# Kernel optimization log

Measured on AMD Instinct MI355X. Metric: run time of the kernel, lower is better.

## Reference

```python
import jax, jax.numpy as jnp
import numpy as np
from jax import lax

T, B, I, H = 512, 64, 1024, 1024
MIN_VAL, MAX_VAL = -1.0, 1.0  # ConstScalarClamp bounds for both hardtanh norm-scales


def setup_inputs() -> dict:
    key = jax.random.key(0)
    ks = jax.random.split(key, 12)
    return {
        "inputs": jax.random.normal(ks[0], (T, B, I), jnp.float32),
        "state": jax.random.normal(ks[1], (B, H), jnp.float32),
        "weight_ri": jax.random.normal(ks[2], (H, I), jnp.float32) * 0.02,
        "weight_ii": jax.random.normal(ks[3], (H, I), jnp.float32) * 0.02,
        "weight_ni": jax.random.normal(ks[4], (H, I), jnp.float32) * 0.02,
        "weight_rh": jax.random.normal(ks[5], (H, H), jnp.float32) * 0.02,
        "weight_ih": jax.random.normal(ks[6], (H, H), jnp.float32) * 0.02,
        "weight_nh": jax.random.normal(ks[7], (H, H), jnp.float32) * 0.02,
        "bias_r": jax.random.normal(ks[8], (H,), jnp.float32) * 0.02,
        "bias_i": jax.random.normal(ks[9], (H,), jnp.float32) * 0.02,
        "bias_ni": jax.random.normal(ks[10], (H,), jnp.float32) * 0.02,
        "bias_nh": jax.random.normal(ks[11], (H,), jnp.float32) * 0.02,
    }


def _clamp(x):
    return jnp.clip(x, MIN_VAL, MAX_VAL)


def reference(inputs, state, weight_ri, weight_ii, weight_ni,
              weight_rh, weight_ih, weight_nh,
              bias_r, bias_i, bias_ni, bias_nh):
    # FP quant type: weight proxies are identity, quant_sigmoid/tanh are plain
    # sigmoid/tanh, and both norm-scale QuantHardTanh ops are clamp to [-1, 1].
    h0 = _clamp(state)  # state = norm_scale_out(state) before the loop

    def step(h, x_t):
        x = _clamp(x_t)  # input_quant = norm_scale_out(inputs[i])
        rgate = jax.nn.sigmoid(x @ weight_ri.T + h @ weight_rh.T + bias_r)
        igate = jax.nn.sigmoid(x @ weight_ii.T + h @ weight_ih.T + bias_i)
        gates_ni = x @ weight_ni.T + bias_ni
        gates_nh = h @ weight_nh.T + bias_nh
        ngate = jnp.tanh(_clamp(gates_ni) + _clamp(rgate * gates_nh))
        s = _clamp(h) - ngate
        hy = ngate + _clamp(igate * s)
        return hy, hy

    last, outputs = lax.scan(step, h0, inputs)
    return outputs, last
```

## Files before the change

### kernel.cpp

```cpp
#include <hip/hip_runtime.h>
#include <hip/hip_bf16.h>
#include <cstdio>


typedef short bf16x8 __attribute__((ext_vector_type(8)));
typedef float f32x4 __attribute__((ext_vector_type(4)));
typedef int i32x4 __attribute__((ext_vector_type(4)));

#define NT 512
#define NB 64
#define NH 1024
#define NBH 65536

#define OFF_HBUF  4096UL
#define OFF_WCAT  (OFF_HBUF + 2UL * NB * NH * 4)
#define OFF_WH    (OFF_WCAT + 3UL * NH * NH * 2)
#define OFF_GR    (OFF_WH   + 3UL * NH * NH * 2)
#define OFF_GI    (OFF_GR   + (unsigned long)NT * NB * NH * 2)
#define WS_NEED   (OFF_GI   + (unsigned long)NT * NB * NH * 2)

__device__ __forceinline__ float clampf(float x) { return fminf(fmaxf(x, -1.f), 1.f); }

__device__ __forceinline__ unsigned short f2bf(float x) {
  __hip_bfloat16 h = __float2bfloat16(x);
  union { __hip_bfloat16 h; unsigned short u; } cv;
  cv.h = h;
  return cv.u;
}
__device__ __forceinline__ float bf2f(unsigned short u) {
  return __uint_as_float(((unsigned)u) << 16);
}
__device__ __forceinline__ float frcp(float x) { return __builtin_amdgcn_rcpf(x); }
__device__ __forceinline__ float fsigmoid(float x) { return frcp(1.f + __expf(-x)); }
__device__ __forceinline__ float ftanh(float z) { return 1.f - 2.f * frcp(1.f + __expf(2.f * z)); }

__device__ __forceinline__ i32x4 pack8(float4 v0, float4 v1) {
  i32x4 q;
  q[0] = (int)(f2bf(clampf(v0.x)) | ((unsigned)f2bf(clampf(v0.y)) << 16));
  q[1] = (int)(f2bf(clampf(v0.z)) | ((unsigned)f2bf(clampf(v0.w)) << 16));
  q[2] = (int)(f2bf(clampf(v1.x)) | ((unsigned)f2bf(clampf(v1.y)) << 16));
  q[3] = (int)(f2bf(clampf(v1.z)) | ((unsigned)f2bf(clampf(v1.w)) << 16));
  return q;
}

__device__ __forceinline__ void load_frags8(const unsigned short* p, i32x4 a[8]) {
  asm volatile(
      "global_load_dwordx4 %0, %8, off\n\t"
      "global_load_dwordx4 %1, %8, off offset:64\n\t"
      "global_load_dwordx4 %2, %8, off offset:128\n\t"
      "global_load_dwordx4 %3, %8, off offset:192\n\t"
      "global_load_dwordx4 %4, %8, off offset:256\n\t"
      "global_load_dwordx4 %5, %8, off offset:320\n\t"
      "global_load_dwordx4 %6, %8, off offset:384\n\t"
      "global_load_dwordx4 %7, %8, off offset:448\n\t"
      "s_waitcnt vmcnt(0)"
      : "=&v"(a[0]), "=&v"(a[1]), "=&v"(a[2]), "=&v"(a[3]),
        "=&v"(a[4]), "=&v"(a[5]), "=&v"(a[6]), "=&v"(a[7])
      : "v"(p)
      : "memory");
}
__device__ __forceinline__ void store_u32_wt(unsigned int* p, unsigned v) {
  asm volatile("global_store_dword %0, %1, off sc0 sc1" :: "v"(p), "v"(v) : "memory");
}

__global__ void k_convert_weights(const float* __restrict__ wri, const float* __restrict__ wii,
                                  const float* __restrict__ wni, const float* __restrict__ wrh,
                                  const float* __restrict__ wih, const float* __restrict__ wnh,
                                  unsigned short* __restrict__ wcat, unsigned short* __restrict__ wh) {
  const long total = 6L * 1024 * 1024;
  long stride = (long)gridDim.x * blockDim.x * 4;
  for (long i = ((long)blockIdx.x * blockDim.x + threadIdx.x) * 4; i < total; i += stride) {
    int m = (int)(i >> 20);
    long off = i & 1048575L;
    const float* srcs[6] = {wri, wii, wni, wrh, wih, wnh};
    float4 v = *(const float4*)(srcs[m] + off);
    ushort4 o;
    o.x = f2bf(v.x); o.y = f2bf(v.y); o.z = f2bf(v.z); o.w = f2bf(v.w);
    unsigned short* dst = (m < 3) ? (wcat + ((long)m << 20) + off)
                                  : (wh + ((long)(m - 3) << 20) + off);
    *(ushort4*)dst = o;
  }
}

#define BK 64
__launch_bounds__(256)
__global__ void k_gemm_x(const float* __restrict__ A,
                         const unsigned short* __restrict__ Bw,
                         unsigned short* __restrict__ gr, unsigned short* __restrict__ gi,
                         float* __restrict__ gni,
                         const float* __restrict__ br, const float* __restrict__ bi,
                         const float* __restrict__ bni) {
  __shared__ unsigned short As[128 * BK];
  __shared__ unsigned short Bs[128 * BK];

  int bid = blockIdx.x;
  int bm = bid / 24, bn = bid % 24;
  int tid = threadIdx.x;
  int lane = tid & 63, w = tid >> 6;
  int wm = w >> 1, wn = w & 1;

  long arow0 = (long)bm * 128;
  long brow0 = (long)bn * 128;

  f32x4 acc[4][4] = {};

  for (int kt = 0; kt < 1024; kt += BK) {
    __syncthreads();
#pragma unroll
    for (int it = 0; it < 4; ++it) {
      int f = it * 2048 + tid * 8;
      int r = f >> 6, c = f & 63;
      const float* ap = A + (arow0 + r) * 1024 + kt + c;
      float4 v0 = *(const float4*)ap;
      float4 v1 = *(const float4*)(ap + 4);
      i32x4 p = pack8(v0, v1);
      *(i32x4*)(&As[f]) = p;
      *(int4*)(&Bs[f]) = *(const int4*)(Bw + (brow0 + r) * 1024 + kt + c);
    }
    __syncthreads();
#pragma unroll
    for (int ks = 0; ks < 2; ++ks) {
      bf16x8 a[4], b[4];
#pragma unroll
      for (int fm = 0; fm < 4; ++fm)
        a[fm] = *(const bf16x8*)(&As[(wm * 64 + fm * 16 + (lane & 15)) * BK + ks * 32 + (lane >> 4) * 8]);
#pragma unroll
      for (int fn = 0; fn < 4; ++fn)
        b[fn] = *(const bf16x8*)(&Bs[(wn * 64 + fn * 16 + (lane & 15)) * BK + ks * 32 + (lane >> 4) * 8]);
#pragma unroll
      for (int fm = 0; fm < 4; ++fm)
#pragma unroll
        for (int fn = 0; fn < 4; ++fn)
          acc[fm][fn] = __builtin_amdgcn_mfma_f32_16x16x32_bf16(a[fm], b[fn], acc[fm][fn], 0, 0, 0);
    }
  }

  int g = bn >> 3;
  const float* bias = (g == 0) ? br : (g == 1) ? bi : bni;
#pragma unroll
  for (int fm = 0; fm < 4; ++fm) {
    long m = arow0 + wm * 64 + fm * 16 + (lane >> 4) * 4;
#pragma unroll
    for (int fn = 0; fn < 4; ++fn) {
      long n = brow0 + wn * 64 + fn * 16 + (lane & 15);
      long colg = n & 1023;
      float bv = bias[colg];
#pragma unroll
      for (int r2 = 0; r2 < 4; ++r2) {
        float v = acc[fm][fn][r2] + bv;
        long idx = (m + r2) * 1024 + colg;
        if (g == 0)      gr[idx] = f2bf(v);
        else if (g == 1) gi[idx] = f2bf(v);
        else             gni[idx] = clampf(v);
      }
    }
  }
}

__launch_bounds__(256, 1)
__global__ void k_recurrent(const unsigned short* __restrict__ wh,
                            const unsigned short* __restrict__ gr,
                            const unsigned short* __restrict__ gi,
                            const float* __restrict__ state,
                            const float* __restrict__ bias_nh,
                            unsigned int* __restrict__ hbuf,
                            float* __restrict__ out) {
  __shared__ unsigned short h_lds[8 * 1024];
  __shared__ float red[4][3][2][8][16];

  int tid = threadIdx.x;
  int lane = tid & 63, w = tid >> 6;
  int wg = blockIdx.x;
  int grp = wg >> 5;
  int slot = wg & 31;

  int klane = (lane >> 4) * 8;
  int k0 = w * 256;
  i32x4 wfi[3][2][8];
#pragma unroll
  for (int g2 = 0; g2 < 3; ++g2)
#pragma unroll
    for (int n2 = 0; n2 < 2; ++n2) {
      int col = slot * 32 + n2 * 16 + (lane & 15);
      load_frags8(wh + ((long)g2 << 20) + (long)col * 1024 + k0 + klane, wfi[g2][n2]);
    }

  int row = tid >> 5, col = tid & 31;
  long cellofs = (long)(grp * 8 + row) * 1024 + slot * 32 + col;
  float h_local = clampf(state[cellofs]);
  float bnh = bias_nh[slot * 32 + col];

#pragma unroll
  for (int c = 0; c < 4; ++c) {
    int m = c * 256 + tid;
    const float* sp = state + (long)grp * 8192 + (long)m * 8;
    float4 v0 = *(const float4*)sp;
    float4 v1 = *(const float4*)(sp + 4);
    int flat = m * 16;
    int r8 = m >> 7;
    *(i32x4*)((char*)h_lds + (flat ^ (r8 << 4))) = pack8(v0, v1);
  }

  const int rowb = (lane & 7) * 2048;
  const int colb = w * 512 + ((lane >> 4) * 16);
  const int rsw = (lane & 7) << 4;

  float grv = bf2f(gr[cellofs]);
  float giv = bf2f(gi[cellofs]);
  float gniv = out[cellofs];

  __syncthreads();

#pragma unroll 1
  for (int t = 0; t < NT; ++t) {
    f32x4 acc[3][2] = {};
#pragma unroll
    for (int s = 0; s < 8; ++s) {
      bf16x8 a = *(const bf16x8*)((const char*)h_lds + rowb + ((colb + s * 64) ^ rsw));
#pragma unroll
      for (int g2 = 0; g2 < 3; ++g2)
#pragma unroll
        for (int n2 = 0; n2 < 2; ++n2)
          acc[g2][n2] = __builtin_amdgcn_mfma_f32_16x16x32_bf16(
              a, __builtin_bit_cast(bf16x8, wfi[g2][n2][s]), acc[g2][n2], 0, 0, 0);
    }

    int rq = lane >> 4;
    if (rq < 2) {
#pragma unroll
      for (int g2 = 0; g2 < 3; ++g2)
#pragma unroll
        for (int n2 = 0; n2 < 2; ++n2)
#pragma unroll
          for (int r = 0; r < 4; ++r)
            red[w][g2][n2][rq * 4 + r][lane & 15] = acc[g2][n2][r];
    }
    __syncthreads();

    int n2c = col >> 4, cc = col & 15;
    float pr = red[0][0][n2c][row][cc] + red[1][0][n2c][row][cc]
             + red[2][0][n2c][row][cc] + red[3][0][n2c][row][cc];
    float pi = red[0][1][n2c][row][cc] + red[1][1][n2c][row][cc]
             + red[2][1][n2c][row][cc] + red[3][1][n2c][row][cc];
    float pn = red[0][2][n2c][row][cc] + red[1][2][n2c][row][cc]
             + red[2][2][n2c][row][cc] + red[3][2][n2c][row][cc];

    float rg = fsigmoid(pr + grv);
    float ig = fsigmoid(pi + giv);
    float ng = ftanh(gniv + clampf(rg * (pn + bnh)));
    float sx = clampf(h_local) - ng;
    float hy = ng + clampf(ig * sx);

    out[(long)t * NBH + cellofs] = hy;
    h_local = hy;

    unsigned tgt = (unsigned)(t + 1);
    long bank = (long)(tgt & 1) * NBH;
    store_u32_wt(hbuf + bank + cellofs, ((unsigned)f2bf(hy) << 16) | tgt);

    if (t + 1 < NT) {
      long g2ofs = (long)tgt * NBH + cellofs;
      grv = bf2f(gr[g2ofs]); giv = bf2f(gi[g2ofs]); gniv = out[g2ofs];

      const unsigned int* base = hbuf + bank + (long)grp * 8192;
      i32x4 d[8];
      for (unsigned it = 0;; ++it) {
#pragma unroll
        for (int c = 0; c < 8; ++c) {
          const unsigned int* p = base + (long)(c * 256 + tid) * 4;
          asm volatile("global_load_dwordx4 %0, %1, off sc0 sc1"
                       : "=&v"(d[c]) : "v"(p) : "memory");
        }
        asm volatile("s_waitcnt vmcnt(0)" ::: "memory");
        unsigned mn = 0xFFFFFFFFu;
#pragma unroll
        for (int c = 0; c < 8; ++c)
#pragma unroll
          for (int e = 0; e < 4; ++e)
            mn = min(mn, ((unsigned)d[c][e]) & 0xFFFFu);
        if (__all((int)(mn >= tgt)) || it > 4096u) break;
        __builtin_amdgcn_s_sleep(2);
      }
#pragma unroll
      for (int c = 0; c < 8; ++c) {
        int n = c * 256 + tid;
        int flat = n * 8;
        int r8 = n >> 8;
        int swz = flat ^ (r8 << 4);
        int2 v;
        v.x = (int)__builtin_amdgcn_perm((unsigned)d[c][1], (unsigned)d[c][0], 0x07060302u);
        v.y = (int)__builtin_amdgcn_perm((unsigned)d[c][3], (unsigned)d[c][2], 0x07060302u);
        *(int2*)((char*)h_lds + swz) = v;
      }
      __syncthreads();
    }
  }

  out[(long)NT * NBH + cellofs] = h_local;
}

extern "C" void kernel_launch(void* const* d_in, const int* in_sizes, int n_in,
                              void* d_out, int out_size, void* d_ws, size_t ws_size,
                              hipStream_t stream) {
  const float* inputs = (const float*)d_in[0];
  const float* state  = (const float*)d_in[1];
  const float* wri = (const float*)d_in[2];
  const float* wii = (const float*)d_in[3];
  const float* wni = (const float*)d_in[4];
  const float* wrh = (const float*)d_in[5];
  const float* wih = (const float*)d_in[6];
  const float* wnh = (const float*)d_in[7];
  const float* br  = (const float*)d_in[8];
  const float* bi  = (const float*)d_in[9];
  const float* bni = (const float*)d_in[10];
  const float* bnh = (const float*)d_in[11];

  if (ws_size < WS_NEED) {
    fprintf(stderr, "kernel_launch: ws too small (%zu < %lu)\n", ws_size, WS_NEED);
    return;
  }

  char* ws = (char*)d_ws;
  unsigned int*   hbuf  = (unsigned int*)(ws + OFF_HBUF);
  unsigned short* wcat  = (unsigned short*)(ws + OFF_WCAT);
  unsigned short* whp   = (unsigned short*)(ws + OFF_WH);
  unsigned short* grw   = (unsigned short*)(ws + OFF_GR);
  unsigned short* giw   = (unsigned short*)(ws + OFF_GI);
  float* out = (float*)d_out;

  hipMemsetAsync(ws, 0, OFF_WCAT, stream);
  k_convert_weights<<<512, 256, 0, stream>>>(wri, wii, wni, wrh, wih, wnh, wcat, whp);
  k_gemm_x<<<6144, 256, 0, stream>>>(inputs, wcat, grw, giw, out, br, bi, bni);
  k_recurrent<<<256, 256, 0, stream>>>(whp, grw, giw, state, bnh, hbuf, out);
}
```

Measured before the change: 1.986 ms.

## Drop per-step barrier via double-buffered reduction and per-chunk flag polling

The recurrent kernel double-buffers the cross-wave reduction array by step parity and removes the trailing __syncthreads after the h exchange. Each wave now polls only the slice of K it consumes, re-issuing loads only for chunks whose step flags are not yet ready. The hbuf flag store moves ahead of the output store, and the pre-GEMM stages the bf16 weight tile through direct global-to-LDS loads. Without the barrier, waves can read h_lds written by other waves, so correctness depends on the new mapping in which each wave writes exactly the K slice it later reads.

```diff
diff --git a/kernel.cpp b/kernel.cpp
--- a/kernel.cpp
+++ b/kernel.cpp
@@ -41,6 +41,12 @@
   q[2] = (int)(f2bf(clampf(v1.x)) | ((unsigned)f2bf(clampf(v1.y)) << 16));
   q[3] = (int)(f2bf(clampf(v1.z)) | ((unsigned)f2bf(clampf(v1.w)) << 16));
   return q;
+}
+
+__device__ __forceinline__ void gload_lds16(const void* g, void* l) {
+  __builtin_amdgcn_global_load_lds(
+      (const __attribute__((address_space(1))) void*)g,
+      (__attribute__((address_space(3))) void*)l, 16, 0, 0);
 }
 
 __device__ __forceinline__ void load_frags8(const unsigned short* p, i32x4 a[8]) {
@@ -110,12 +116,11 @@
     for (int it = 0; it < 4; ++it) {
       int f = it * 2048 + tid * 8;
       int r = f >> 6, c = f & 63;
+      gload_lds16(Bw + (brow0 + r) * 1024 + kt + c, &Bs[f]);
       const float* ap = A + (arow0 + r) * 1024 + kt + c;
       float4 v0 = *(const float4*)ap;
       float4 v1 = *(const float4*)(ap + 4);
-      i32x4 p = pack8(v0, v1);
-      *(i32x4*)(&As[f]) = p;
-      *(int4*)(&Bs[f]) = *(const int4*)(Bw + (brow0 + r) * 1024 + kt + c);
+      *(i32x4*)(&As[f]) = pack8(v0, v1);
     }
     __syncthreads();
 #pragma unroll
@@ -166,7 +171,7 @@
                             unsigned int* __restrict__ hbuf,
                             float* __restrict__ out) {
   __shared__ unsigned short h_lds[8 * 1024];
-  __shared__ float red[4][3][2][8][16];
+  __shared__ float red[2][4][3][2][8][16];
 
   int tid = threadIdx.x;
   int lane = tid & 63, w = tid >> 6;
@@ -191,14 +196,14 @@
   float bnh = bias_nh[slot * 32 + col];
 
 #pragma unroll
-  for (int c = 0; c < 4; ++c) {
-    int m = c * 256 + tid;
-    const float* sp = state + (long)grp * 8192 + (long)m * 8;
-    float4 v0 = *(const float4*)sp;
-    float4 v1 = *(const float4*)(sp + 4);
-    int flat = m * 16;
-    int r8 = m >> 7;
-    *(i32x4*)((char*)h_lds + (flat ^ (r8 << 4))) = pack8(v0, v1);
+  for (int c = 0; c < 8; ++c) {
+    const float* sp = state + (long)(grp * 8 + c) * 1024 + k0 + lane * 4;
+    float4 v = *(const float4*)sp;
+    int2 pv;
+    pv.x = (int)(f2bf(clampf(v.x)) | ((unsigned)f2bf(clampf(v.y)) << 16));
+    pv.y = (int)(f2bf(clampf(v.z)) | ((unsigned)f2bf(clampf(v.w)) << 16));
+    int flat = c * 2048 + (k0 + lane * 4) * 2;
+    *(int2*)((char*)h_lds + (flat ^ (c << 4))) = pv;
   }
 
   const int rowb = (lane & 7) * 2048;
@@ -213,6 +218,7 @@
 
 #pragma unroll 1
   for (int t = 0; t < NT; ++t) {
+    int par = t & 1;
     f32x4 acc[3][2] = {};
 #pragma unroll
     for (int s = 0; s < 8; ++s) {
@@ -233,17 +239,17 @@
         for (int n2 = 0; n2 < 2; ++n2)
 #pragma unroll
           for (int r = 0; r < 4; ++r)
-            red[w][g2][n2][rq * 4 + r][lane & 15] = acc[g2][n2][r];
+            red[par][w][g2][n2][rq * 4 + r][lane & 15] = acc[g2][n2][r];
     }
     __syncthreads();
 
     int n2c = col >> 4, cc = col & 15;
-    float pr = red[0][0][n2c][row][cc] + red[1][0][n2c][row][cc]
-             + red[2][0][n2c][row][cc] + red[3][0][n2c][row][cc];
-    float pi = red[0][1][n2c][row][cc] + red[1][1][n2c][row][cc]
-             + red[2][1][n2c][row][cc] + red[3][1][n2c][row][cc];
-    float pn = red[0][2][n2c][row][cc] + red[1][2][n2c][row][cc]
-             + red[2][2][n2c][row][cc] + red[3][2][n2c][row][cc];
+    float pr = red[par][0][0][n2c][row][cc] + red[par][1][0][n2c][row][cc]
+             + red[par][2][0][n2c][row][cc] + red[par][3][0][n2c][row][cc];
+    float pi = red[par][0][1][n2c][row][cc] + red[par][1][1][n2c][row][cc]
+             + red[par][2][1][n2c][row][cc] + red[par][3][1][n2c][row][cc];
+    float pn = red[par][0][2][n2c][row][cc] + red[par][1][2][n2c][row][cc]
+             + red[par][2][2][n2c][row][cc] + red[par][3][2][n2c][row][cc];
 
     float rg = fsigmoid(pr + grv);
     float ig = fsigmoid(pi + giv);
@@ -251,48 +257,45 @@
     float sx = clampf(h_local) - ng;
     float hy = ng + clampf(ig * sx);
 
-    out[(long)t * NBH + cellofs] = hy;
-    h_local = hy;
-
     unsigned tgt = (unsigned)(t + 1);
     long bank = (long)(tgt & 1) * NBH;
     store_u32_wt(hbuf + bank + cellofs, ((unsigned)f2bf(hy) << 16) | tgt);
+    out[(long)t * NBH + cellofs] = hy;
+    h_local = hy;
 
     if (t + 1 < NT) {
       long g2ofs = (long)tgt * NBH + cellofs;
       grv = bf2f(gr[g2ofs]); giv = bf2f(gi[g2ofs]); gniv = out[g2ofs];
 
-      const unsigned int* base = hbuf + bank + (long)grp * 8192;
+      const unsigned int* base = hbuf + bank + (long)grp * 8192 + k0 + lane * 4;
       i32x4 d[8];
-      for (unsigned it = 0;; ++it) {
-#pragma unroll
-        for (int c = 0; c < 8; ++c) {
-          const unsigned int* p = base + (long)(c * 256 + tid) * 4;
-          asm volatile("global_load_dwordx4 %0, %1, off sc0 sc1"
-                       : "=&v"(d[c]) : "v"(p) : "memory");
-        }
+      unsigned done = 0;
+      for (unsigned it2 = 0;; ++it2) {
+#pragma unroll
+        for (int c = 0; c < 8; ++c)
+          if (!((done >> c) & 1)) {
+            asm volatile("global_load_dwordx4 %0, %1, off sc0 sc1"
+                         : "=v"(d[c]) : "v"(base + c * 1024) : "memory");
+          }
         asm volatile("s_waitcnt vmcnt(0)" ::: "memory");
-        unsigned mn = 0xFFFFFFFFu;
 #pragma unroll
         for (int c = 0; c < 8; ++c)
-#pragma unroll
-          for (int e = 0; e < 4; ++e)
-            mn = min(mn, ((unsigned)d[c][e]) & 0xFFFFu);
-        if (__all((int)(mn >= tgt)) || it > 4096u) break;
-        __builtin_amdgcn_s_sleep(2);
+          if (!((done >> c) & 1)) {
+            unsigned m0 = min((unsigned)d[c][0] & 0xFFFFu, (unsigned)d[c][1] & 0xFFFFu);
+            unsigned m1 = min((unsigned)d[c][2] & 0xFFFFu, (unsigned)d[c][3] & 0xFFFFu);
+            if (min(m0, m1) >= tgt) done |= (1u << c);
+          }
+        if (__all((int)(done == 0xFFu)) || it2 > 8192u) break;
+        __builtin_amdgcn_s_sleep(1);
       }
 #pragma unroll
       for (int c = 0; c < 8; ++c) {
-        int n = c * 256 + tid;
-        int flat = n * 8;
-        int r8 = n >> 8;
-        int swz = flat ^ (r8 << 4);
+        int flat = c * 2048 + (k0 + lane * 4) * 2;
         int2 v;
         v.x = (int)__builtin_amdgcn_perm((unsigned)d[c][1], (unsigned)d[c][0], 0x07060302u);
         v.y = (int)__builtin_amdgcn_perm((unsigned)d[c][3], (unsigned)d[c][2], 0x07060302u);
-        *(int2*)((char*)h_lds + swz) = v;
+        *(int2*)((char*)h_lds + (flat ^ (c << 4))) = v;
       }
-      __syncthreads();
     }
   }
 
```

Result: no change. 1.998 ms (+0.6%).
